# Optimization experiments

Hardware: AMD Instinct MI355X
Metric: run time of the kernel (lower is better)

The kernel has to match this reference:

```python
import jax, jax.numpy as jnp
import numpy as np

# rp = [l1, l2] link parameters (stand-in for the repo's robot-parameter object)
RP = jnp.array([1.0, 1.0], dtype=jnp.float32)
EPS = 1e-8


def _mlp(x, w1, b1, w2, b2, w3, b3):
    # Linear(2,16) -> Softplus -> Linear(16,16) -> Softplus -> Linear(16,2)
    h = jax.nn.softplus(x @ w1.T + b1)
    h = jax.nn.softplus(h @ w2.T + b2)
    return h @ w3.T + b3


def _analytic_theta_0(qi):
    # smooth analytic coordinate (stand-in for transforms.analytic_theta_0)
    return RP[0] * jnp.arctan2(qi[1], qi[0])


def _analytic_theta_1(qi):
    return RP[1] * jnp.sqrt(qi[0] ** 2 + qi[1] ** 2 + EPS)


def setup_inputs() -> dict:
    key = jax.random.key(0)
    ks = jax.random.split(key, 13)
    N = 1_000_000
    q = jax.random.normal(ks[0], (N, 2), dtype=jnp.float32)

    def lin(k, out_d, in_d):
        kw, kb = jax.random.split(k)
        s = 1.0 / np.sqrt(in_d)
        w = jax.random.uniform(kw, (out_d, in_d), jnp.float32, -s, s)
        b = jax.random.uniform(kb, (out_d,), jnp.float32, -s, s)
        return w, b

    enc_w1, enc_b1 = lin(ks[1], 16, 2)
    enc_w2, enc_b2 = lin(ks[2], 16, 16)
    enc_w3, enc_b3 = lin(ks[3], 2, 16)
    dec_w1, dec_b1 = lin(ks[4], 16, 2)
    dec_w2, dec_b2 = lin(ks[5], 16, 16)
    dec_w3, dec_b3 = lin(ks[6], 2, 16)
    return dict(q=q,
                enc_w1=enc_w1, enc_b1=enc_b1, enc_w2=enc_w2, enc_b2=enc_b2,
                enc_w3=enc_w3, enc_b3=enc_b3,
                dec_w1=dec_w1, dec_b1=dec_b1, dec_w2=dec_w2, dec_b2=dec_b2,
                dec_w3=dec_w3, dec_b3=dec_b3)


def reference(q, enc_w1, enc_b1, enc_w2, enc_b2, enc_w3, enc_b3,
              dec_w1, dec_b1, dec_w2, dec_b2, dec_w3, dec_b3):
    enc = lambda x: _mlp(x, enc_w1, enc_b1, enc_w2, enc_b2, enc_w3, enc_b3)
    dec = lambda x: _mlp(x, dec_w1, dec_b1, dec_w2, dec_b2, dec_w3, dec_b3)

    # analytic jacobians (per-sample fn returns shape (1,) like unsqueeze(0))
    def f0(qi):
        t = jnp.expand_dims(_analytic_theta_0(qi), 0)
        return t, t

    def f1(qi):
        t = jnp.expand_dims(_analytic_theta_1(qi), 0)
        return t, t

    J0, _ = jax.vmap(jax.jacfwd(f0, has_aux=True))(q)  # [N,1,2]
    J1, _ = jax.vmap(jax.jacfwd(f1, has_aux=True))(q)  # [N,1,2]
    J_h_ana = jnp.concatenate([J0, J1], axis=1).astype(jnp.float32)  # [N,2,2]

    theta = enc(q)                                  # [N,2]
    J_h = jax.vmap(jax.jacfwd(enc))(q)              # [N,2,2]
    q_hat = dec(theta)                              # [N,2]
    J_h_dec = jax.vmap(jax.jacfwd(dec))(theta)      # [N,2,2]
    return theta, J_h, q_hat, J_h_dec, J_h_ana
```

## Files before the change

kernel.cpp:

```cpp
#include <hip/hip_runtime.h>
#include <math.h>


typedef float  f32x4  __attribute__((ext_vector_type(4)));
typedef short  bf16x4 __attribute__((ext_vector_type(4)));

__device__ __forceinline__ unsigned short f2bf1(float f) {
    unsigned u = __builtin_bit_cast(unsigned, f);
    u += 0x7FFFu + ((u >> 16) & 1u);
    return (unsigned short)(u >> 16);
}

__device__ __forceinline__ unsigned packbf(float a, float b) {
    return __builtin_amdgcn_perm(__builtin_bit_cast(unsigned, b),
                                 __builtin_bit_cast(unsigned, a), 0x07060302u);
}

__device__ __forceinline__ bf16x4 pack4(float a, float b, float c, float d) {
    union { unsigned u[2]; bf16x4 f; } x;
    x.u[0] = packbf(a, b); x.u[1] = packbf(c, d);
    return x.f;
}

__device__ __forceinline__ f32x4 mfma16(bf16x4 a, bf16x4 b, f32x4 c) {
#if __has_builtin(__builtin_amdgcn_mfma_f32_16x16x16bf16_1k)
    return __builtin_amdgcn_mfma_f32_16x16x16bf16_1k(a, b, c, 0, 0, 0);
#else
    f32x4 d;
    asm("v_mfma_f32_16x16x16_bf16 %0, %1, %2, %3"
        : "=&v"(d) : "v"(a), "v"(b), "v"(c));
    return d;
#endif
}

__device__ __forceinline__ void activ(float z, float& sp, float& sg) {
    float t = __expf(-z);
    sg = __builtin_amdgcn_rcpf(1.0f + t);
    sp = fmaf(-0.69314718056f, __log2f(sg), z);
}

__global__ void prep_kernel(
    const float* __restrict__ ew1, const float* __restrict__ eb1,
    const float* __restrict__ ew2, const float* __restrict__ eb2,
    const float* __restrict__ ew3,
    const float* __restrict__ dw1, const float* __restrict__ db1,
    const float* __restrict__ dw2, const float* __restrict__ db2,
    const float* __restrict__ dw3,
    float* __restrict__ ws)
{
    const int t = threadIdx.x;
    if (t >= 64) return;
    const int g = t >> 4, m = t & 15;
    unsigned short* frag = (unsigned short*)(ws + 2048);
#pragma unroll
    for (int j = 0; j < 4; ++j) {
        const int i = g * 4 + j;
        ws[t*12 + j]           = ew1[2*i];
        ws[t*12 + 4 + j]       = ew1[2*i + 1];
        ws[t*12 + 8 + j]       = eb1[i];
        ws[768 + t*12 + j]     = dw1[2*i];
        ws[768 + t*12 + 4 + j] = dw1[2*i + 1];
        ws[768 + t*12 + 8 + j] = db1[i];
        ws[1536 + t*4 + j]     = eb2[i];
        ws[1792 + t*4 + j]     = db2[i];
        frag[t*4 + j]       = f2bf1(ew2[m*16 + i]);
        frag[512 + t*4 + j] = f2bf1(dw2[m*16 + i]);
        const int r3 = m & 3;
        frag[256 + t*4 + j] = (r3 < 2) ? f2bf1(ew3[r3*16 + i]) : (unsigned short)0;
        frag[768 + t*4 + j] = (r3 < 2) ? f2bf1(dw3[r3*16 + i]) : (unsigned short)0;
    }
}

__device__ __forceinline__ void mlp16(
    f32x4 Wa, f32x4 Wb, f32x4 Bb, f32x4 B2c,
    bf16x4 A2, bf16x4 A3, f32x4 C3, f32x4 Z,
    float x, float y,
    float& o0, float& o1, float& J00, float& J01, float& J10, float& J11)
{
    float h0, h1, h2, h3, ta0, ta1, ta2, ta3, tb0, tb1, tb2, tb3;
    {
        float z, sp, sg;
        z = fmaf(Wa[0], x, fmaf(Wb[0], y, Bb[0])); activ(z, sp, sg);
        h0 = sp; ta0 = sg * Wa[0]; tb0 = sg * Wb[0];
        z = fmaf(Wa[1], x, fmaf(Wb[1], y, Bb[1])); activ(z, sp, sg);
        h1 = sp; ta1 = sg * Wa[1]; tb1 = sg * Wb[1];
        z = fmaf(Wa[2], x, fmaf(Wb[2], y, Bb[2])); activ(z, sp, sg);
        h2 = sp; ta2 = sg * Wa[2]; tb2 = sg * Wb[2];
        z = fmaf(Wa[3], x, fmaf(Wb[3], y, Bb[3])); activ(z, sp, sg);
        h3 = sp; ta3 = sg * Wa[3]; tb3 = sg * Wb[3];
    }
    f32x4 zc = mfma16(A2, pack4(h0,  h1,  h2,  h3),  B2c);
    f32x4 ua = mfma16(A2, pack4(ta0, ta1, ta2, ta3), Z);
    f32x4 ub = mfma16(A2, pack4(tb0, tb1, tb2, tb3), Z);

    float g0, g1, g2, g3, sa0, sa1, sa2, sa3, sb0, sb1, sb2, sb3;
    {
        float sp, sg;
        activ(zc[0], sp, sg); g0 = sp; sa0 = sg * ua[0]; sb0 = sg * ub[0];
        activ(zc[1], sp, sg); g1 = sp; sa1 = sg * ua[1]; sb1 = sg * ub[1];
        activ(zc[2], sp, sg); g2 = sp; sa2 = sg * ua[2]; sb2 = sg * ub[2];
        activ(zc[3], sp, sg); g3 = sp; sa3 = sg * ua[3]; sb3 = sg * ub[3];
    }
    f32x4 oz = mfma16(A3, pack4(g0,  g1,  g2,  g3),  C3);
    f32x4 oa = mfma16(A3, pack4(sa0, sa1, sa2, sa3), Z);
    f32x4 ob = mfma16(A3, pack4(sb0, sb1, sb2, sb3), Z);
    o0 = oz[0]; o1 = oz[1];
    J00 = oa[0]; J10 = oa[1]; J01 = ob[0]; J11 = ob[1];
}

__global__ __launch_bounds__(256) void ae_mfma_kernel(
    const float* __restrict__ q,
    const float* __restrict__ eb3, const float* __restrict__ db3,
    const float* __restrict__ ws, float* __restrict__ out, int n)
{
    const int lane = threadIdx.x & 63;
    const int wv = blockIdx.x * 4 + (threadIdx.x >> 6);
    const int g = lane >> 4, m16 = lane & 15;
    const long base = (long)wv * 64;
    if (base >= n) return;

    const f32x4 eWa = *(const f32x4*)(ws + (size_t)lane*12);
    const f32x4 eWb = *(const f32x4*)(ws + (size_t)lane*12 + 4);
    const f32x4 eBb = *(const f32x4*)(ws + (size_t)lane*12 + 8);
    const f32x4 dWa = *(const f32x4*)(ws + 768 + (size_t)lane*12);
    const f32x4 dWb = *(const f32x4*)(ws + 768 + (size_t)lane*12 + 4);
    const f32x4 dBb = *(const f32x4*)(ws + 768 + (size_t)lane*12 + 8);
    const f32x4 eB2 = *(const f32x4*)(ws + 1536 + (size_t)lane*4);
    const f32x4 dB2 = *(const f32x4*)(ws + 1792 + (size_t)lane*4);
    const bf16x4* fr = (const bf16x4*)(ws + 2048);
    const bf16x4 A2e = fr[lane],       A3e = fr[64 + lane];
    const bf16x4 A2d = fr[128 + lane], A3d = fr[192 + lane];
    f32x4 C3e; C3e[0] = eb3[0]; C3e[1] = eb3[1]; C3e[2] = 0.0f; C3e[3] = 0.0f;
    f32x4 C3d; C3d[0] = db3[0]; C3d[1] = db3[1]; C3d[2] = 0.0f; C3d[3] = 0.0f;
    f32x4 Z;   Z[0] = 0.0f; Z[1] = 0.0f; Z[2] = 0.0f; Z[3] = 0.0f;

    const size_t nn = (size_t)n;

#define LOADXY(c, xc, yc)                                                   \
    float xc, yc;                                                           \
    {                                                                       \
        long s_ = base + (c)*16 + m16;                                      \
        long si_ = s_ < n ? s_ : (long)n - 1;                               \
        const float2 qv_ = ((const float2*)q)[si_];                         \
        xc = qv_.x; yc = qv_.y;                                             \
    }

#define ENC(c, xc, yc)                                                      \
    float t0_##c, t1_##c, E00_##c, E01_##c, E10_##c, E11_##c;               \
    mlp16(eWa, eWb, eBb, eB2, A2e, A3e, C3e, Z, xc, yc,                     \
          t0_##c, t1_##c, E00_##c, E01_##c, E10_##c, E11_##c);

#define DEC_STORE(c, xc, yc)                                                \
    {                                                                       \
        float q0_, q1_, D00_, D01_, D10_, D11_;                             \
        mlp16(dWa, dWb, dBb, dB2, A2d, A3d, C3d, Z, t0_##c, t1_##c,         \
              q0_, q1_, D00_, D01_, D10_, D11_);                            \
        long sp_ = base + (c)*16 + m16;                                     \
        if (g == (c) && sp_ < n) {                                          \
            float r2_ = fmaf(xc, xc, yc * yc);                              \
            float iv_ = __builtin_amdgcn_rcpf(r2_);                         \
            float rv_ = __builtin_amdgcn_rsqf(r2_ + 1e-8f);                 \
            ((float2*)(out))[sp_]          = make_float2(t0_##c, t1_##c);   \
            ((float4*)(out + 2*nn))[sp_]   = make_float4(E00_##c, E01_##c,  \
                                                         E10_##c, E11_##c); \
            ((float2*)(out + 6*nn))[sp_]   = make_float2(q0_, q1_);         \
            ((float4*)(out + 8*nn))[sp_]   = make_float4(D00_, D01_,        \
                                                         D10_, D11_);       \
            ((float4*)(out + 12*nn))[sp_]  = make_float4(-yc * iv_, xc * iv_,\
                                                         xc * rv_, yc * rv_);\
        }                                                                   \
    }

    LOADXY(0, x0, y0) LOADXY(1, x1, y1) LOADXY(2, x2, y2) LOADXY(3, x3, y3)

    ENC(0, x0, y0)
    ENC(1, x1, y1)
    DEC_STORE(0, x0, y0)
    ENC(2, x2, y2)
    DEC_STORE(1, x1, y1)
    ENC(3, x3, y3)
    DEC_STORE(2, x2, y2)
    DEC_STORE(3, x3, y3)

#undef LOADXY
#undef ENC
#undef DEC_STORE
}

extern "C" void kernel_launch(void* const* d_in, const int* in_sizes, int n_in,
                              void* d_out, int out_size, void* d_ws, size_t ws_size,
                              hipStream_t stream)
{
    const float* q   = (const float*)d_in[0];
    const float* ew1 = (const float*)d_in[1];
    const float* eb1 = (const float*)d_in[2];
    const float* ew2 = (const float*)d_in[3];
    const float* eb2 = (const float*)d_in[4];
    const float* ew3 = (const float*)d_in[5];
    const float* eb3 = (const float*)d_in[6];
    const float* dw1 = (const float*)d_in[7];
    const float* db1 = (const float*)d_in[8];
    const float* dw2 = (const float*)d_in[9];
    const float* db2 = (const float*)d_in[10];
    const float* dw3 = (const float*)d_in[11];
    const float* db3 = (const float*)d_in[12];

    const int n = in_sizes[0] / 2;
    float* ws = (float*)d_ws;

    prep_kernel<<<1, 64, 0, stream>>>(ew1, eb1, ew2, eb2, ew3,
                                      dw1, db1, dw2, db2, dw3, ws);

    const int waves  = (n + 63) / 64;
    const int blocks = (waves + 3) / 4;
    ae_mfma_kernel<<<blocks, 256, 0, stream>>>(q, eb3, db3, ws, (float*)d_out, n);
}
```

Before: 127.3 us.

## Fold log2e/ln2 into weights and precompute W2*W1 fragments to cut VALU work

Scales the first-layer and second-layer biases and weights by log2(e) in the prep kernel so softplus and sigmoid use the native exp2/log2 directly, and folds ln2 into the output-layer value fragment. The first-layer Jacobian products are precomputed as W2*diag(W1 column) bf16 fragments, so the per-sample sigmoid vector is packed once and shared by both Jacobian MFMAs instead of forming and packing two scaled vectors. Adds a launch_bounds occupancy hint. This trims per-sample transcendental and multiply work at the cost of more fragment registers and extra bf16 rounding of the premultiplied weights.

```diff
diff --git a/kernel.cpp b/kernel.cpp
--- a/kernel.cpp
+++ b/kernel.cpp
@@ -4,6 +4,9 @@
 
 typedef float  f32x4  __attribute__((ext_vector_type(4)));
 typedef short  bf16x4 __attribute__((ext_vector_type(4)));
+
+#define LOG2E 1.44269504089f
+#define LN2   0.69314718056f
 
 __device__ __forceinline__ unsigned short f2bf1(float f) {
     unsigned u = __builtin_bit_cast(unsigned, f);
@@ -33,10 +36,12 @@
 #endif
 }
 
-__device__ __forceinline__ void activ(float z, float& sp, float& sg) {
-    float t = __expf(-z);
-    sg = __builtin_amdgcn_rcpf(1.0f + t);
-    sp = fmaf(-0.69314718056f, __log2f(sg), z);
+__device__ __forceinline__ float exp2neg(float z) {
+#if __has_builtin(__builtin_amdgcn_exp2f)
+    return __builtin_amdgcn_exp2f(-z);
+#else
+    float r; asm("v_exp_f32 %0, -%1" : "=v"(r) : "v"(z)); return r;
+#endif
 }
 
 __global__ void prep_kernel(
@@ -55,60 +60,81 @@
 #pragma unroll
     for (int j = 0; j < 4; ++j) {
         const int i = g * 4 + j;
-        ws[t*12 + j]           = ew1[2*i];
-        ws[t*12 + 4 + j]       = ew1[2*i + 1];
-        ws[t*12 + 8 + j]       = eb1[i];
-        ws[768 + t*12 + j]     = dw1[2*i];
-        ws[768 + t*12 + 4 + j] = dw1[2*i + 1];
-        ws[768 + t*12 + 8 + j] = db1[i];
-        ws[1536 + t*4 + j]     = eb2[i];
-        ws[1792 + t*4 + j]     = db2[i];
-        frag[t*4 + j]       = f2bf1(ew2[m*16 + i]);
-        frag[512 + t*4 + j] = f2bf1(dw2[m*16 + i]);
+        const float ewa = ew1[2*i], ewb = ew1[2*i+1];
+        const float dwa = dw1[2*i], dwb = dw1[2*i+1];
+        ws[t*12 + j]           = ewa * LOG2E;
+        ws[t*12 + 4 + j]       = ewb * LOG2E;
+        ws[t*12 + 8 + j]       = eb1[i] * LOG2E;
+        ws[768 + t*12 + j]     = dwa * LOG2E;
+        ws[768 + t*12 + 4 + j] = dwb * LOG2E;
+        ws[768 + t*12 + 8 + j] = db1[i] * LOG2E;
+        ws[1536 + t*4 + j]     = eb2[i] * LOG2E;
+        ws[1792 + t*4 + j]     = db2[i] * LOG2E;
+        const float e2 = ew2[m*16 + i], d2 = dw2[m*16 + i];
+        frag[0*256 + t*4 + j] = f2bf1(e2);
+        frag[1*256 + t*4 + j] = f2bf1(e2 * ewa);
+        frag[2*256 + t*4 + j] = f2bf1(e2 * ewb);
+        frag[5*256 + t*4 + j] = f2bf1(d2);
+        frag[6*256 + t*4 + j] = f2bf1(d2 * dwa);
+        frag[7*256 + t*4 + j] = f2bf1(d2 * dwb);
         const int r3 = m & 3;
-        frag[256 + t*4 + j] = (r3 < 2) ? f2bf1(ew3[r3*16 + i]) : (unsigned short)0;
-        frag[768 + t*4 + j] = (r3 < 2) ? f2bf1(dw3[r3*16 + i]) : (unsigned short)0;
+        const float e3 = (r3 < 2) ? ew3[r3*16 + i] : 0.0f;
+        const float d3 = (r3 < 2) ? dw3[r3*16 + i] : 0.0f;
+        frag[3*256 + t*4 + j] = f2bf1(e3 * LN2);
+        frag[4*256 + t*4 + j] = f2bf1(e3);
+        frag[8*256 + t*4 + j] = f2bf1(d3 * LN2);
+        frag[9*256 + t*4 + j] = f2bf1(d3);
     }
 }
 
 __device__ __forceinline__ void mlp16(
     f32x4 Wa, f32x4 Wb, f32x4 Bb, f32x4 B2c,
-    bf16x4 A2, bf16x4 A3, f32x4 C3, f32x4 Z,
+    bf16x4 A2, bf16x4 A2a, bf16x4 A2b, bf16x4 A3v, bf16x4 A3j,
+    f32x4 C3, f32x4 Z,
     float x, float y,
     float& o0, float& o1, float& J00, float& J01, float& J10, float& J11)
 {
-    float h0, h1, h2, h3, ta0, ta1, ta2, ta3, tb0, tb1, tb2, tb3;
+    float h0, h1, h2v, h3, s0, s1, s2, s3;
     {
-        float z, sp, sg;
-        z = fmaf(Wa[0], x, fmaf(Wb[0], y, Bb[0])); activ(z, sp, sg);
-        h0 = sp; ta0 = sg * Wa[0]; tb0 = sg * Wb[0];
-        z = fmaf(Wa[1], x, fmaf(Wb[1], y, Bb[1])); activ(z, sp, sg);
-        h1 = sp; ta1 = sg * Wa[1]; tb1 = sg * Wb[1];
-        z = fmaf(Wa[2], x, fmaf(Wb[2], y, Bb[2])); activ(z, sp, sg);
-        h2 = sp; ta2 = sg * Wa[2]; tb2 = sg * Wb[2];
-        z = fmaf(Wa[3], x, fmaf(Wb[3], y, Bb[3])); activ(z, sp, sg);
-        h3 = sp; ta3 = sg * Wa[3]; tb3 = sg * Wb[3];
-    }
-    f32x4 zc = mfma16(A2, pack4(h0,  h1,  h2,  h3),  B2c);
-    f32x4 ua = mfma16(A2, pack4(ta0, ta1, ta2, ta3), Z);
-    f32x4 ub = mfma16(A2, pack4(tb0, tb1, tb2, tb3), Z);
+        float z, t, w;
+        z = fmaf(Wa[0], x, fmaf(Wb[0], y, Bb[0]));
+        t = exp2neg(z); w = 1.0f + t;
+        s0 = __builtin_amdgcn_rcpf(w); h0 = z + __log2f(w);
+        z = fmaf(Wa[1], x, fmaf(Wb[1], y, Bb[1]));
+        t = exp2neg(z); w = 1.0f + t;
+        s1 = __builtin_amdgcn_rcpf(w); h1 = z + __log2f(w);
+        z = fmaf(Wa[2], x, fmaf(Wb[2], y, Bb[2]));
+        t = exp2neg(z); w = 1.0f + t;
+        s2 = __builtin_amdgcn_rcpf(w); h2v = z + __log2f(w);
+        z = fmaf(Wa[3], x, fmaf(Wb[3], y, Bb[3]));
+        t = exp2neg(z); w = 1.0f + t;
+        s3 = __builtin_amdgcn_rcpf(w); h3 = z + __log2f(w);
+    }
+    const bf16x4 Bsg = pack4(s0, s1, s2, s3);
+    f32x4 zc = mfma16(A2,  pack4(h0, h1, h2v, h3), B2c);
+    f32x4 ua = mfma16(A2a, Bsg, Z);
+    f32x4 ub = mfma16(A2b, Bsg, Z);
 
     float g0, g1, g2, g3, sa0, sa1, sa2, sa3, sb0, sb1, sb2, sb3;
     {
-        float sp, sg;
-        activ(zc[0], sp, sg); g0 = sp; sa0 = sg * ua[0]; sb0 = sg * ub[0];
-        activ(zc[1], sp, sg); g1 = sp; sa1 = sg * ua[1]; sb1 = sg * ub[1];
-        activ(zc[2], sp, sg); g2 = sp; sa2 = sg * ua[2]; sb2 = sg * ub[2];
-        activ(zc[3], sp, sg); g3 = sp; sa3 = sg * ua[3]; sb3 = sg * ub[3];
-    }
-    f32x4 oz = mfma16(A3, pack4(g0,  g1,  g2,  g3),  C3);
-    f32x4 oa = mfma16(A3, pack4(sa0, sa1, sa2, sa3), Z);
-    f32x4 ob = mfma16(A3, pack4(sb0, sb1, sb2, sb3), Z);
+        float t, w, r;
+        t = exp2neg(zc[0]); w = 1.0f + t; r = __builtin_amdgcn_rcpf(w);
+        g0 = zc[0] + __log2f(w); sa0 = r * ua[0]; sb0 = r * ub[0];
+        t = exp2neg(zc[1]); w = 1.0f + t; r = __builtin_amdgcn_rcpf(w);
+        g1 = zc[1] + __log2f(w); sa1 = r * ua[1]; sb1 = r * ub[1];
+        t = exp2neg(zc[2]); w = 1.0f + t; r = __builtin_amdgcn_rcpf(w);
+        g2 = zc[2] + __log2f(w); sa2 = r * ua[2]; sb2 = r * ub[2];
+        t = exp2neg(zc[3]); w = 1.0f + t; r = __builtin_amdgcn_rcpf(w);
+        g3 = zc[3] + __log2f(w); sa3 = r * ua[3]; sb3 = r * ub[3];
+    }
+    f32x4 oz = mfma16(A3v, pack4(g0,  g1,  g2,  g3),  C3);
+    f32x4 oa = mfma16(A3j, pack4(sa0, sa1, sa2, sa3), Z);
+    f32x4 ob = mfma16(A3j, pack4(sb0, sb1, sb2, sb3), Z);
     o0 = oz[0]; o1 = oz[1];
     J00 = oa[0]; J10 = oa[1]; J01 = ob[0]; J11 = ob[1];
 }
 
-__global__ __launch_bounds__(256) void ae_mfma_kernel(
+__global__ __launch_bounds__(256, 4) void ae_mfma_kernel(
     const float* __restrict__ q,
     const float* __restrict__ eb3, const float* __restrict__ db3,
     const float* __restrict__ ws, float* __restrict__ out, int n)
@@ -128,8 +154,12 @@
     const f32x4 eB2 = *(const f32x4*)(ws + 1536 + (size_t)lane*4);
     const f32x4 dB2 = *(const f32x4*)(ws + 1792 + (size_t)lane*4);
     const bf16x4* fr = (const bf16x4*)(ws + 2048);
-    const bf16x4 A2e = fr[lane],       A3e = fr[64 + lane];
-    const bf16x4 A2d = fr[128 + lane], A3d = fr[192 + lane];
+    const bf16x4 A2e  = fr[0*64 + lane], A2ae = fr[1*64 + lane];
+    const bf16x4 A2be = fr[2*64 + lane];
+    const bf16x4 A3ve = fr[3*64 + lane], A3je = fr[4*64 + lane];
+    const bf16x4 A2d  = fr[5*64 + lane], A2ad = fr[6*64 + lane];
+    const bf16x4 A2bd = fr[7*64 + lane];
+    const bf16x4 A3vd = fr[8*64 + lane], A3jd = fr[9*64 + lane];
     f32x4 C3e; C3e[0] = eb3[0]; C3e[1] = eb3[1]; C3e[2] = 0.0f; C3e[3] = 0.0f;
     f32x4 C3d; C3d[0] = db3[0]; C3d[1] = db3[1]; C3d[2] = 0.0f; C3d[3] = 0.0f;
     f32x4 Z;   Z[0] = 0.0f; Z[1] = 0.0f; Z[2] = 0.0f; Z[3] = 0.0f;
@@ -147,14 +177,14 @@
 
 #define ENC(c, xc, yc)                                                      \
     float t0_##c, t1_##c, E00_##c, E01_##c, E10_##c, E11_##c;               \
-    mlp16(eWa, eWb, eBb, eB2, A2e, A3e, C3e, Z, xc, yc,                     \
+    mlp16(eWa, eWb, eBb, eB2, A2e, A2ae, A2be, A3ve, A3je, C3e, Z, xc, yc,  \
           t0_##c, t1_##c, E00_##c, E01_##c, E10_##c, E11_##c);
 
 #define DEC_STORE(c, xc, yc)                                                \
     {                                                                       \
         float q0_, q1_, D00_, D01_, D10_, D11_;                             \
-        mlp16(dWa, dWb, dBb, dB2, A2d, A3d, C3d, Z, t0_##c, t1_##c,         \
-              q0_, q1_, D00_, D01_, D10_, D11_);                            \
+        mlp16(dWa, dWb, dBb, dB2, A2d, A2ad, A2bd, A3vd, A3jd, C3d, Z,      \
+              t0_##c, t1_##c, q0_, q1_, D00_, D01_, D10_, D11_);            \
         long sp_ = base + (c)*16 + m16;                                     \
         if (g == (c) && sp_ < n) {                                          \
             float r2_ = fmaf(xc, xc, yc * yc);                              \
```

After: 121.9 us. -4.3%, faster.
